# Optimization experiments

Measured on AMD Instinct MI355X. Metric: run time of the kernel, lower is better.

The kernel has to match this reference:

```python
import math
import jax, jax.numpy as jnp
import numpy as np

N, L, H, E, K = 4, 768, 8, 64, 1  # batch, seq (L==S), heads, feat, num_sines


def setup_inputs() -> dict:
    key = jax.random.key(0)
    ks = jax.random.split(key, 8)
    queries = jax.random.normal(ks[0], (N, L, H, E), jnp.float32)
    keys = jax.random.normal(ks[1], (N, L, H, E), jnp.float32)
    values = jax.random.normal(ks[2], (N, L, H, E), jnp.float32)
    attn_mask_add = jnp.zeros((L, L), jnp.float32)
    key_lengths_add = jnp.zeros((N, L), jnp.float32)
    freqs = jax.random.normal(ks[3], (H, E, K), jnp.float32) - 4.0  # init shift
    offsets = jax.random.normal(ks[4], (H, E, K), jnp.float32)
    gains = jax.random.normal(ks[5], (H, E, K), jnp.float32)
    # gains.data /= sqrt(||gains||_{-1}) / 2
    gains = gains / (jnp.sqrt(jnp.linalg.norm(gains, axis=-1, keepdims=True)) / 2.0)
    gate = jax.random.normal(ks[6], (H, E), jnp.float32)
    return dict(queries=queries, keys=keys, values=values,
                attn_mask_add=attn_mask_add, key_lengths_add=key_lengths_add,
                freqs=freqs, offsets=offsets, gains=gains, gate=gate)


def reference(queries, keys, values, attn_mask_add, key_lengths_add,
              freqs, offsets, gains, gate):
    n, l, h, e = queries.shape
    softmax_temp = 1.0 / math.sqrt(e)
    positions = jnp.arange(l, dtype=queries.dtype)  # (L,)
    f = jax.nn.sigmoid(freqs)[None] / 2.0  # (1,H,E,K)
    phases_q = 2.0 * math.pi * f * positions[:, None, None, None] + offsets[None]
    phases_k = 2.0 * math.pi * f * positions[:, None, None, None]
    # interleave cos/sin along last dim -> (L,H,E,2K)
    omega_q = jnp.stack([jnp.cos(phases_q), jnp.sin(phases_q)], axis=-1).reshape(l, h, e, 2 * f.shape[-1])
    omega_k = jnp.stack([jnp.cos(phases_k), jnp.sin(phases_k)], axis=-1).reshape(l, h, e, 2 * f.shape[-1])
    g = jax.nn.softplus(gains)
    g2 = jnp.stack([g, g], axis=-1).reshape(h, e, 2 * f.shape[-1])  # (H,E,2K)
    # positional kernel P: (L,S,H,E)
    P = jnp.einsum('lhdk,hdk,shdk->lshd', omega_q, g2 ** 2, omega_k)
    P = (1.0 - gate) * P + gate  # gated
    QK = jnp.einsum('nlhd,lshd,nshd->nhls', queries, P, keys)
    QK = QK + attn_mask_add[None, None] + key_lengths_add[:, None, None, :]
    A = jax.nn.softmax(softmax_temp * QK, axis=-1)
    V = jnp.einsum('nhls,nshd->nlhd', A, values)
    return V
```

## Files before the change

### kernel.cpp

```cpp
#include <hip/hip_runtime.h>
#include <math.h>
#include <stdint.h>

#define NB 4
#define LQ 768
#define NH 8
#define NE 64
#define ND 192
#define TEMP 0.125f

typedef _Float16 f16;
typedef __attribute__((ext_vector_type(8))) _Float16 f16x8;
typedef __attribute__((ext_vector_type(4))) float f32x4;

__device__ __forceinline__ void stage16(f16* lds_base, const f16* g, int lane) {
#if __has_builtin(__builtin_amdgcn_global_load_lds)
    __builtin_amdgcn_global_load_lds(
        (const __attribute__((address_space(1))) uint32_t*)g,
        (__attribute__((address_space(3))) uint32_t*)lds_base, 16, 0, 0);
#else
    *(uint4*)((char*)lds_base + lane * 16) = *(const uint4*)g;
#endif
}

__global__ __launch_bounds__(256) void sinattn_prep(
    const float* __restrict__ Q, const float* __restrict__ K,
    const float* __restrict__ freqs, const float* __restrict__ offsets,
    const float* __restrict__ gains, const float* __restrict__ gate,
    f16* __restrict__ Qf, f16* __restrict__ Kf)
{
    int idx = blockIdx.x * 256 + threadIdx.x;
    int eg = idx & 7, e0 = eg << 3;
    int h  = (idx >> 3) & 7;
    int t  = idx >> 6;
    int l  = t % LQ;
    int n  = t / LQ;
    int nh = (n << 3) | h;
    int he = (h << 6) | e0;

    const float* qp = Q + (size_t)idx * 8;
    const float* kp = K + (size_t)idx * 8;
    float4 q0 = *(const float4*)qp, q1 = *(const float4*)(qp + 4);
    float4 k0 = *(const float4*)kp, k1 = *(const float4*)(kp + 4);
    float qv[8] = {q0.x,q0.y,q0.z,q0.w, q1.x,q1.y,q1.z,q1.w};
    float kv[8] = {k0.x,k0.y,k0.z,k0.w, k1.x,k1.y,k1.z,k1.w};

    float4 fA = *(const float4*)(freqs   + he), fB = *(const float4*)(freqs   + he + 4);
    float4 oA = *(const float4*)(offsets + he), oB = *(const float4*)(offsets + he + 4);
    float4 gA = *(const float4*)(gains   + he), gB = *(const float4*)(gains   + he + 4);
    float4 tA = *(const float4*)(gate    + he), tB = *(const float4*)(gate    + he + 4);
    float fv[8] = {fA.x,fA.y,fA.z,fA.w, fB.x,fB.y,fB.z,fB.w};
    float ov[8] = {oA.x,oA.y,oA.z,oA.w, oB.x,oB.y,oB.z,oB.w};
    float gv[8] = {gA.x,gA.y,gA.z,gA.w, gB.x,gB.y,gB.z,gB.w};
    float tv[8] = {tA.x,tA.y,tA.z,tA.w, tB.x,tB.y,tB.z,tB.w};

    f16x8 oq0, oq1, oq2, ok0, ok1, ok2;
    float lf = (float)l;
    #pragma unroll
    for (int j = 0; j < 8; ++j) {
        float f  = 0.5f / (1.0f + __expf(-fv[j]));
        float gn = gv[j];
        float sp = (gn > 15.0f) ? gn : __logf(1.0f + __expf(gn));
        float gt = tv[j];
        float a  = (1.0f - gt) * sp * sp;
        float fh = __uint_as_float(__float_as_uint(f) & 0xFFFFF000u);
        float fl = f - fh;
        float t0 = lf * fh;
        float tr = t0 - floorf(t0);
        tr = __builtin_fmaf(lf, fl, tr);
        float pk = 6.28318530717958647f * tr;
        float pq = pk + ov[j];
        float sq = __sinf(pq), cq = __cosf(pq);
        float sk = __sinf(pk), ck = __cosf(pk);
        oq0[j] = (f16)(qv[j] * a * cq);
        oq1[j] = (f16)(qv[j] * a * sq);
        oq2[j] = (f16)(qv[j] * gt);
        ok0[j] = (f16)(kv[j] * ck);
        ok1[j] = (f16)(kv[j] * sk);
        ok2[j] = (f16)(kv[j]);
    }
    size_t base = ((size_t)nh * LQ + l) * ND + e0;
    *(f16x8*)(Qf + base)            = oq0;
    *(f16x8*)(Qf + base + NE)       = oq1;
    *(f16x8*)(Qf + base + 2 * NE)   = oq2;
    *(f16x8*)(Kf + base)            = ok0;
    *(f16x8*)(Kf + base + NE)       = ok1;
    *(f16x8*)(Kf + base + 2 * NE)   = ok2;
}

__global__ __launch_bounds__(256) void sinattn_vt(
    const float* __restrict__ V, f16* __restrict__ Vt)
{
    __shared__ f16 tile[64][72];
    int b = blockIdx.x;
    int st = b % 12, nh = b / 12;
    int n = nh >> 3, h = nh & 7;
    int s0 = st * 64;
    int tid = threadIdx.x;

    int sl = tid >> 2, e0 = (tid & 3) << 4;
    const float4* vp = (const float4*)(V + ((size_t)(n * LQ + s0 + sl) * NH + h) * NE + e0);
    float4 a0 = vp[0], a1 = vp[1], a2 = vp[2], a3 = vp[3];
    float vv[16] = { a0.x,a0.y,a0.z,a0.w, a1.x,a1.y,a1.z,a1.w,
                     a2.x,a2.y,a2.z,a2.w, a3.x,a3.y,a3.z,a3.w };
    #pragma unroll
    for (int j = 0; j < 16; ++j) tile[e0 + j][sl] = (f16)vv[j];
    __syncthreads();

    int er = tid >> 2, sc = tid & 3;
    f16* op = Vt + ((size_t)nh * NE + er) * LQ + s0 + sc * 16;
    *(uint4*)op       = *(const uint4*)&tile[er][sc * 16];
    *(uint4*)(op + 8) = *(const uint4*)&tile[er][sc * 16 + 8];
}

__global__ __launch_bounds__(256, 2) void sinattn_flash(
    const f16* __restrict__ Qf, const f16* __restrict__ Kf, const f16* __restrict__ Vt,
    const float* __restrict__ mask, const float* __restrict__ keylen,
    float* __restrict__ out)
{
    __shared__ __attribute__((aligned(16))) f16 sK[2][64 * 24 * 8];
    __shared__ __attribute__((aligned(16))) f16 sV[2][64 * 8 * 8];
    __shared__ __attribute__((aligned(16))) f16 sP[4][16 * 72];

    int tid  = threadIdx.x;
    int wv   = tid >> 6;
    int lane = tid & 63;
    int grp  = lane >> 4;
    int r16  = lane & 15;
    int swz  = r16 & 7;

    int bid = blockIdx.x;
    int nh  = bid & 31;
    int lt  = bid >> 5;
    int n   = nh >> 3;
    int l0  = lt * 64;

    f16x8 qf[6];
    {
        size_t rbase = ((size_t)nh * LQ + l0 + wv * 16 + r16) * ND + grp * 8;
        #pragma unroll
        for (int d0 = 0; d0 < 6; ++d0)
            qf[d0] = *(const f16x8*)(Qf + rbase + d0 * 32);
    }

    int goffK[6], goffV[2];
    #pragma unroll
    for (int i = 0; i < 6; ++i) {
        int p = i * 256 + wv * 64 + lane;
        int r = p / 24, c = p - r * 24;
        int cl = (c & ~7) | ((c & 7) ^ (r & 7));
        goffK[i] = r * ND + cl * 8;
    }
    #pragma unroll
    for (int i = 0; i < 2; ++i) {
        int p = i * 256 + wv * 64 + lane;
        int r = p >> 3, c = p & 7;
        goffV[i] = r * LQ + (c ^ (r & 7)) * 8;
    }
    const f16* Kb = Kf + (size_t)nh * LQ * ND;
    const f16* Vb = Vt + (size_t)nh * NE * LQ;

    {
        #pragma unroll
        for (int i = 0; i < 6; ++i)
            stage16(&sK[0][(i * 256 + wv * 64) * 8], Kb + goffK[i], lane);
        #pragma unroll
        for (int i = 0; i < 2; ++i)
            stage16(&sV[0][(i * 256 + wv * 64) * 8], Vb + goffV[i], lane);
    }

    float m_i[4], l_i[4];
    f32x4 O[4];
    #pragma unroll
    for (int rr = 0; rr < 4; ++rr) { m_i[rr] = -INFINITY; l_i[rr] = 0.f; }
    #pragma unroll
    for (int tt = 0; tt < 4; ++tt)
        #pragma unroll
        for (int rr = 0; rr < 4; ++rr) O[tt][rr] = 0.f;

    for (int c = 0; c < 12; ++c) {
        int cur = c & 1;
        int s0  = c * 64;
        __syncthreads();

        if (c < 11) {
            const f16* kg = Kb + (s0 + 64) * ND;
            const f16* vg = Vb + (s0 + 64);
            #pragma unroll
            for (int i = 0; i < 6; ++i)
                stage16(&sK[cur ^ 1][(i * 256 + wv * 64) * 8], kg + goffK[i], lane);
            #pragma unroll
            for (int i = 0; i < 2; ++i)
                stage16(&sV[cur ^ 1][(i * 256 + wv * 64) * 8], vg + goffV[i], lane);
        }

        float klv[4], mreg[4][4];
        #pragma unroll
        for (int j = 0; j < 4; ++j) klv[j] = keylen[n * LQ + s0 + j * 16 + r16];
        #pragma unroll
        for (int rr = 0; rr < 4; ++rr) {
            int lrow = l0 + wv * 16 + grp * 4 + rr;
            #pragma unroll
            for (int j = 0; j < 4; ++j)
                mreg[rr][j] = mask[lrow * LQ + s0 + j * 16 + r16];
        }

        f32x4 st[4];
        #pragma unroll
        for (int j = 0; j < 4; ++j)
            #pragma unroll
            for (int rr = 0; rr < 4; ++rr) st[j][rr] = 0.f;
        #pragma unroll
        for (int d0 = 0; d0 < 6; ++d0) {
            #pragma unroll
            for (int j = 0; j < 4; ++j) {
                int cc = d0 * 4 + grp;
                int cl = (cc & ~7) | ((cc & 7) ^ swz);
                f16x8 bf = *(const f16x8*)&sK[cur][((j * 16 + r16) * 24 + cl) * 8];
                st[j] = __builtin_amdgcn_mfma_f32_16x16x32_f16(qf[d0], bf, st[j], 0, 0, 0);
            }
        }

        #pragma unroll
        for (int rr = 0; rr < 4; ++rr) {
            float lg[4];
            float mx = -INFINITY;
            #pragma unroll
            for (int j = 0; j < 4; ++j) {
                lg[j] = TEMP * (st[j][rr] + mreg[rr][j] + klv[j]);
                mx = fmaxf(mx, lg[j]);
            }
            #pragma unroll
            for (int d = 1; d < 16; d <<= 1) mx = fmaxf(mx, __shfl_xor(mx, d));
            float mnew  = fmaxf(m_i[rr], mx);
            float alpha = __expf(m_i[rr] - mnew);
            float rs = 0.f;
            #pragma unroll
            for (int j = 0; j < 4; ++j) {
                float p = __expf(lg[j] - mnew);
                rs += p;
                sP[wv][(grp * 4 + rr) * 72 + j * 16 + r16] = (f16)p;
            }
            #pragma unroll
            for (int d = 1; d < 16; d <<= 1) rs += __shfl_xor(rs, d);
            l_i[rr] = l_i[rr] * alpha + rs;
            m_i[rr] = mnew;
            #pragma unroll
            for (int tt = 0; tt < 4; ++tt) O[tt][rr] *= alpha;
        }

        #pragma unroll
        for (int kk = 0; kk < 2; ++kk) {
            f16x8 pa = *(const f16x8*)&sP[wv][r16 * 72 + kk * 32 + grp * 8];
            #pragma unroll
            for (int tt = 0; tt < 4; ++tt) {
                int cc = kk * 4 + grp;
                f16x8 vb = *(const f16x8*)&sV[cur][((tt * 16 + r16) * 8 + (cc ^ swz)) * 8];
                O[tt] = __builtin_amdgcn_mfma_f32_16x16x32_f16(pa, vb, O[tt], 0, 0, 0);
            }
        }
    }

    #pragma unroll
    for (int rr = 0; rr < 4; ++rr) {
        float inv = 1.0f / l_i[rr];
        int lrow = l0 + wv * 16 + grp * 4 + rr;
        float* op = out + ((size_t)(n * LQ + lrow) * NH + (nh & 7)) * NE;
        #pragma unroll
        for (int tt = 0; tt < 4; ++tt)
            op[tt * 16 + r16] = O[tt][rr] * inv;
    }
}

extern "C" void kernel_launch(void* const* d_in, const int* in_sizes, int n_in,
                              void* d_out, int out_size, void* d_ws, size_t ws_size,
                              hipStream_t stream)
{
    const float* Q      = (const float*)d_in[0];
    const float* K      = (const float*)d_in[1];
    const float* V      = (const float*)d_in[2];
    const float* mask   = (const float*)d_in[3];
    const float* keylen = (const float*)d_in[4];
    const float* freqs  = (const float*)d_in[5];
    const float* offs   = (const float*)d_in[6];
    const float* gains  = (const float*)d_in[7];
    const float* gate   = (const float*)d_in[8];
    float* out = (float*)d_out;

    const size_t P = (size_t)NB * NH * LQ * ND;
    f16* Qf = (f16*)d_ws;
    f16* Kf = Qf + P;
    f16* Vt = Kf + P;

    sinattn_prep<<<768, 256, 0, stream>>>(Q, K, freqs, offs, gains, gate, Qf, Kf);
    sinattn_vt<<<384, 256, 0, stream>>>(V, Vt);
    sinattn_flash<<<NB * NH * (LQ / 64), 256, 0, stream>>>(Qf, Kf, Vt,
                                                           mask, keylen, out);
}
```

Baseline: 122.3 us.

## Split flash attention over key halves with merge kernel; fuse prep and V transpose

```diff
diff --git a/kernel.cpp b/kernel.cpp
--- a/kernel.cpp
+++ b/kernel.cpp
@@ -23,100 +23,99 @@
 #endif
 }
 
-__global__ __launch_bounds__(256) void sinattn_prep(
+__global__ __launch_bounds__(256) void sinattn_prepvt(
     const float* __restrict__ Q, const float* __restrict__ K,
+    const float* __restrict__ V,
     const float* __restrict__ freqs, const float* __restrict__ offsets,
     const float* __restrict__ gains, const float* __restrict__ gate,
-    f16* __restrict__ Qf, f16* __restrict__ Kf)
+    f16* __restrict__ Qf, f16* __restrict__ Kf, f16* __restrict__ Vt)
 {
-    int idx = blockIdx.x * 256 + threadIdx.x;
-    int eg = idx & 7, e0 = eg << 3;
-    int h  = (idx >> 3) & 7;
-    int t  = idx >> 6;
-    int l  = t % LQ;
-    int n  = t / LQ;
-    int nh = (n << 3) | h;
-    int he = (h << 6) | e0;
-
-    const float* qp = Q + (size_t)idx * 8;
-    const float* kp = K + (size_t)idx * 8;
-    float4 q0 = *(const float4*)qp, q1 = *(const float4*)(qp + 4);
-    float4 k0 = *(const float4*)kp, k1 = *(const float4*)(kp + 4);
-    float qv[8] = {q0.x,q0.y,q0.z,q0.w, q1.x,q1.y,q1.z,q1.w};
-    float kv[8] = {k0.x,k0.y,k0.z,k0.w, k1.x,k1.y,k1.z,k1.w};
-
-    float4 fA = *(const float4*)(freqs   + he), fB = *(const float4*)(freqs   + he + 4);
-    float4 oA = *(const float4*)(offsets + he), oB = *(const float4*)(offsets + he + 4);
-    float4 gA = *(const float4*)(gains   + he), gB = *(const float4*)(gains   + he + 4);
-    float4 tA = *(const float4*)(gate    + he), tB = *(const float4*)(gate    + he + 4);
-    float fv[8] = {fA.x,fA.y,fA.z,fA.w, fB.x,fB.y,fB.z,fB.w};
-    float ov[8] = {oA.x,oA.y,oA.z,oA.w, oB.x,oB.y,oB.z,oB.w};
-    float gv[8] = {gA.x,gA.y,gA.z,gA.w, gB.x,gB.y,gB.z,gB.w};
-    float tv[8] = {tA.x,tA.y,tA.z,tA.w, tB.x,tB.y,tB.z,tB.w};
-
-    f16x8 oq0, oq1, oq2, ok0, ok1, ok2;
-    float lf = (float)l;
-    #pragma unroll
-    for (int j = 0; j < 8; ++j) {
-        float f  = 0.5f / (1.0f + __expf(-fv[j]));
-        float gn = gv[j];
-        float sp = (gn > 15.0f) ? gn : __logf(1.0f + __expf(gn));
-        float gt = tv[j];
-        float a  = (1.0f - gt) * sp * sp;
-        float fh = __uint_as_float(__float_as_uint(f) & 0xFFFFF000u);
-        float fl = f - fh;
-        float t0 = lf * fh;
-        float tr = t0 - floorf(t0);
-        tr = __builtin_fmaf(lf, fl, tr);
-        float pk = 6.28318530717958647f * tr;
-        float pq = pk + ov[j];
-        float sq = __sinf(pq), cq = __cosf(pq);
-        float sk = __sinf(pk), ck = __cosf(pk);
-        oq0[j] = (f16)(qv[j] * a * cq);
-        oq1[j] = (f16)(qv[j] * a * sq);
-        oq2[j] = (f16)(qv[j] * gt);
-        ok0[j] = (f16)(kv[j] * ck);
-        ok1[j] = (f16)(kv[j] * sk);
-        ok2[j] = (f16)(kv[j]);
-    }
-    size_t base = ((size_t)nh * LQ + l) * ND + e0;
-    *(f16x8*)(Qf + base)            = oq0;
-    *(f16x8*)(Qf + base + NE)       = oq1;
-    *(f16x8*)(Qf + base + 2 * NE)   = oq2;
-    *(f16x8*)(Kf + base)            = ok0;
-    *(f16x8*)(Kf + base + NE)       = ok1;
-    *(f16x8*)(Kf + base + 2 * NE)   = ok2;
-}
-
-__global__ __launch_bounds__(256) void sinattn_vt(
-    const float* __restrict__ V, f16* __restrict__ Vt)
-{
-    __shared__ f16 tile[64][72];
-    int b = blockIdx.x;
-    int st = b % 12, nh = b / 12;
-    int n = nh >> 3, h = nh & 7;
-    int s0 = st * 64;
-    int tid = threadIdx.x;
-
-    int sl = tid >> 2, e0 = (tid & 3) << 4;
-    const float4* vp = (const float4*)(V + ((size_t)(n * LQ + s0 + sl) * NH + h) * NE + e0);
-    float4 a0 = vp[0], a1 = vp[1], a2 = vp[2], a3 = vp[3];
-    float vv[16] = { a0.x,a0.y,a0.z,a0.w, a1.x,a1.y,a1.z,a1.w,
-                     a2.x,a2.y,a2.z,a2.w, a3.x,a3.y,a3.z,a3.w };
-    #pragma unroll
-    for (int j = 0; j < 16; ++j) tile[e0 + j][sl] = (f16)vv[j];
-    __syncthreads();
-
-    int er = tid >> 2, sc = tid & 3;
-    f16* op = Vt + ((size_t)nh * NE + er) * LQ + s0 + sc * 16;
-    *(uint4*)op       = *(const uint4*)&tile[er][sc * 16];
-    *(uint4*)(op + 8) = *(const uint4*)&tile[er][sc * 16 + 8];
+    if (blockIdx.x < 768) {
+        int idx = blockIdx.x * 256 + threadIdx.x;
+        int eg = idx & 7, e0 = eg << 3;
+        int h  = (idx >> 3) & 7;
+        int t  = idx >> 6;
+        int l  = t % LQ;
+        int n  = t / LQ;
+        int nh = (n << 3) | h;
+        int he = (h << 6) | e0;
+
+        const float* qp = Q + (size_t)idx * 8;
+        const float* kp = K + (size_t)idx * 8;
+        float4 q0 = *(const float4*)qp, q1 = *(const float4*)(qp + 4);
+        float4 k0 = *(const float4*)kp, k1 = *(const float4*)(kp + 4);
+        float qv[8] = {q0.x,q0.y,q0.z,q0.w, q1.x,q1.y,q1.z,q1.w};
+        float kv[8] = {k0.x,k0.y,k0.z,k0.w, k1.x,k1.y,k1.z,k1.w};
+
+        float4 fA = *(const float4*)(freqs   + he), fB = *(const float4*)(freqs   + he + 4);
+        float4 oA = *(const float4*)(offsets + he), oB = *(const float4*)(offsets + he + 4);
+        float4 gA = *(const float4*)(gains   + he), gB = *(const float4*)(gains   + he + 4);
+        float4 tA = *(const float4*)(gate    + he), tB = *(const float4*)(gate    + he + 4);
+        float fv[8] = {fA.x,fA.y,fA.z,fA.w, fB.x,fB.y,fB.z,fB.w};
+        float ov[8] = {oA.x,oA.y,oA.z,oA.w, oB.x,oB.y,oB.z,oB.w};
+        float gv[8] = {gA.x,gA.y,gA.z,gA.w, gB.x,gB.y,gB.z,gB.w};
+        float tv[8] = {tA.x,tA.y,tA.z,tA.w, tB.x,tB.y,tB.z,tB.w};
+
+        f16x8 oq0, oq1, oq2, ok0, ok1, ok2;
+        float lf = (float)l;
+        #pragma unroll
+        for (int j = 0; j < 8; ++j) {
+            float f  = 0.5f / (1.0f + __expf(-fv[j]));
+            float gn = gv[j];
+            float sp = (gn > 15.0f) ? gn : __logf(1.0f + __expf(gn));
+            float gt = tv[j];
+            float a  = (1.0f - gt) * sp * sp;
+            float fh = __uint_as_float(__float_as_uint(f) & 0xFFFFF000u);
+            float fl = f - fh;
+            float t0 = lf * fh;
+            float tr = t0 - floorf(t0);
+            tr = __builtin_fmaf(lf, fl, tr);
+            float pk = 6.28318530717958647f * tr;
+            float pq = pk + ov[j];
+            float sq = __sinf(pq), cq = __cosf(pq);
+            float sk = __sinf(pk), ck = __cosf(pk);
+            oq0[j] = (f16)(qv[j] * a * cq);
+            oq1[j] = (f16)(qv[j] * a * sq);
+            oq2[j] = (f16)(qv[j] * gt);
+            ok0[j] = (f16)(kv[j] * ck);
+            ok1[j] = (f16)(kv[j] * sk);
+            ok2[j] = (f16)(kv[j]);
+        }
+        size_t base = ((size_t)nh * LQ + l) * ND + e0;
+        *(f16x8*)(Qf + base)          = oq0;
+        *(f16x8*)(Qf + base + NE)     = oq1;
+        *(f16x8*)(Qf + base + 2*NE)   = oq2;
+        *(f16x8*)(Kf + base)          = ok0;
+        *(f16x8*)(Kf + base + NE)     = ok1;
+        *(f16x8*)(Kf + base + 2*NE)   = ok2;
+    } else {
+        __shared__ f16 tile[64][72];
+        int b = blockIdx.x - 768;
+        int st = b % 12, nh = b / 12;
+        int n = nh >> 3, h = nh & 7;
+        int s0 = st * 64;
+        int tid = threadIdx.x;
+
+        int sl = tid >> 2, e0 = (tid & 3) << 4;
+        const float4* vp = (const float4*)(V + ((size_t)(n * LQ + s0 + sl) * NH + h) * NE + e0);
+        float4 a0 = vp[0], a1 = vp[1], a2 = vp[2], a3 = vp[3];
+        float vv[16] = { a0.x,a0.y,a0.z,a0.w, a1.x,a1.y,a1.z,a1.w,
+                         a2.x,a2.y,a2.z,a2.w, a3.x,a3.y,a3.z,a3.w };
+        #pragma unroll
+        for (int j = 0; j < 16; ++j) tile[e0 + j][sl] = (f16)vv[j];
+        __syncthreads();
+
+        int er = tid >> 2, sc = tid & 3;
+        f16* op = Vt + ((size_t)nh * NE + er) * LQ + s0 + sc * 16;
+        *(uint4*)op       = *(const uint4*)&tile[er][sc * 16];
+        *(uint4*)(op + 8) = *(const uint4*)&tile[er][sc * 16 + 8];
+    }
 }
 
 __global__ __launch_bounds__(256, 2) void sinattn_flash(
     const f16* __restrict__ Qf, const f16* __restrict__ Kf, const f16* __restrict__ Vt,
     const float* __restrict__ mask, const float* __restrict__ keylen,
-    float* __restrict__ out)
+    float* __restrict__ Op, float* __restrict__ Mp, float* __restrict__ Lp)
 {
     __shared__ __attribute__((aligned(16))) f16 sK[2][64 * 24 * 8];
     __shared__ __attribute__((aligned(16))) f16 sV[2][64 * 8 * 8];
@@ -124,16 +123,20 @@
 
     int tid  = threadIdx.x;
     int wv   = tid >> 6;
+    int wvu  = __builtin_amdgcn_readfirstlane(wv);
     int lane = tid & 63;
     int grp  = lane >> 4;
     int r16  = lane & 15;
     int swz  = r16 & 7;
 
-    int bid = blockIdx.x;
-    int nh  = bid & 31;
-    int lt  = bid >> 5;
-    int n   = nh >> 3;
-    int l0  = lt * 64;
+    int bid  = blockIdx.x;
+    int nh   = bid & 31;
+    int rr2  = bid >> 5;
+    int lt   = rr2 >> 1;
+    int half = rr2 & 1;
+    int n    = nh >> 3;
+    int l0   = lt * 64;
+    int c0   = half * 6;
 
     f16x8 qf[6];
     {
@@ -161,12 +164,14 @@
     const f16* Vb = Vt + (size_t)nh * NE * LQ;
 
     {
+        const f16* kg = Kb + c0 * 64 * ND;
+        const f16* vg = Vb + c0 * 64;
         #pragma unroll
         for (int i = 0; i < 6; ++i)
-            stage16(&sK[0][(i * 256 + wv * 64) * 8], Kb + goffK[i], lane);
+            stage16(&sK[0][(i * 256 + wvu * 64) * 8], kg + goffK[i], lane);
         #pragma unroll
         for (int i = 0; i < 2; ++i)
-            stage16(&sV[0][(i * 256 + wv * 64) * 8], Vb + goffV[i], lane);
+            stage16(&sV[0][(i * 256 + wvu * 64) * 8], vg + goffV[i], lane);
     }
 
     float m_i[4], l_i[4];
@@ -178,20 +183,20 @@
         #pragma unroll
         for (int rr = 0; rr < 4; ++rr) O[tt][rr] = 0.f;
 
-    for (int c = 0; c < 12; ++c) {
+    for (int c = c0; c < c0 + 6; ++c) {
         int cur = c & 1;
         int s0  = c * 64;
         __syncthreads();
 
-        if (c < 11) {
+        if (c < c0 + 5) {
             const f16* kg = Kb + (s0 + 64) * ND;
             const f16* vg = Vb + (s0 + 64);
             #pragma unroll
             for (int i = 0; i < 6; ++i)
-                stage16(&sK[cur ^ 1][(i * 256 + wv * 64) * 8], kg + goffK[i], lane);
+                stage16(&sK[cur ^ 1][(i * 256 + wvu * 64) * 8], kg + goffK[i], lane);
             #pragma unroll
             for (int i = 0; i < 2; ++i)
-                stage16(&sV[cur ^ 1][(i * 256 + wv * 64) * 8], vg + goffV[i], lane);
+                stage16(&sV[cur ^ 1][(i * 256 + wvu * 64) * 8], vg + goffV[i], lane);
         }
 
         float klv[4], mreg[4][4];
@@ -263,13 +268,42 @@
 
     #pragma unroll
     for (int rr = 0; rr < 4; ++rr) {
-        float inv = 1.0f / l_i[rr];
         int lrow = l0 + wv * 16 + grp * 4 + rr;
-        float* op = out + ((size_t)(n * LQ + lrow) * NH + (nh & 7)) * NE;
+        size_t prow = (size_t)(half * 32 + nh) * LQ + lrow;
+        float* op = Op + prow * NE;
         #pragma unroll
         for (int tt = 0; tt < 4; ++tt)
-            op[tt * 16 + r16] = O[tt][rr] * inv;
-    }
+            op[tt * 16 + r16] = O[tt][rr];
+        if (r16 == 0) {
+            Mp[prow] = m_i[rr];
+            Lp[prow] = l_i[rr];
+        }
+    }
+}
+
+__global__ __launch_bounds__(256) void sinattn_merge(
+    const float* __restrict__ Op, const float* __restrict__ Mp,
+    const float* __restrict__ Lp, float* __restrict__ out)
+{
+    int idx = blockIdx.x * 256 + threadIdx.x;
+    if (idx >= NB * LQ * NH * NE) return;
+    int e = idx & 63;
+    int h = (idx >> 6) & 7;
+    int t = idx >> 9;
+    int l = t % LQ;
+    int n = t / LQ;
+    int nh = (n << 3) | h;
+    int row = nh * LQ + l;
+    const int HOFF = 32 * LQ;
+
+    float m0 = Mp[row],        m1 = Mp[HOFF + row];
+    float l0 = Lp[row],        l1 = Lp[HOFF + row];
+    float mm = fmaxf(m0, m1);
+    float a0 = __expf(m0 - mm), a1 = __expf(m1 - mm);
+    float denom = l0 * a0 + l1 * a1;
+    float o0 = Op[(size_t)row * NE + e];
+    float o1 = Op[(size_t)(HOFF + row) * NE + e];
+    out[idx] = (o0 * a0 + o1 * a1) / denom;
 }
 
 extern "C" void kernel_launch(void* const* d_in, const int* in_sizes, int n_in,
@@ -291,9 +325,12 @@
     f16* Qf = (f16*)d_ws;
     f16* Kf = Qf + P;
     f16* Vt = Kf + P;
-
-    sinattn_prep<<<768, 256, 0, stream>>>(Q, K, freqs, offs, gains, gate, Qf, Kf);
-    sinattn_vt<<<384, 256, 0, stream>>>(V, Vt);
-    sinattn_flash<<<NB * NH * (LQ / 64), 256, 0, stream>>>(Qf, Kf, Vt,
-                                                           mask, keylen, out);
-}
+    float* Op = (float*)(Vt + (size_t)NB * NH * NE * LQ);
+    float* Mp = Op + (size_t)2 * 32 * LQ * NE;
+    float* Lp = Mp + (size_t)2 * 32 * LQ;
+
+    sinattn_prepvt<<<1152, 256, 0, stream>>>(Q, K, V, freqs, offs, gains, gate,
+                                             Qf, Kf, Vt);
+    sinattn_flash<<<768, 256, 0, stream>>>(Qf, Kf, Vt, mask, keylen, Op, Mp, Lp);
+    sinattn_merge<<<6144, 256, 0, stream>>>(Op, Mp, Lp, out);
+}
```

After: 122.8 us. About the same (+0.4%).
